# Kernel tuning notes

Measured on AMD Instinct MI355X. Metric: run time of the kernel, lower is better.

Reference implementation:

```python
import jax, jax.numpy as jnp
import numpy as np

SHIFT = 8  # shift_range init kwarg
EPS = 1e-12  # F.normalize default eps (x / max(||x||, eps))


def setup_inputs() -> dict:
    key = jax.random.key(0)
    k1, k2 = jax.random.split(key)
    grd_feature = jax.random.normal(k1, (64, 64, 24, 24), dtype=jnp.float32)
    sat_feature = jax.random.normal(k2, (64, 64, 64, 64), dtype=jnp.float32)
    return {"grd_feature": grd_feature, "sat_feature": sat_feature}


def reference(grd_feature, sat_feature):
    M, C, Hs, Ws = sat_feature.shape
    N, _, H, W = grd_feature.shape
    kH = min(H, Hs - 2 * SHIFT, 24)
    kW = min(W, Ws - 2 * SHIFT, 24)
    # center-crop ground features to kernel size
    grd = grd_feature[:, :, H // 2 - kH // 2: H // 2 + kH // 2,
                      W // 2 - kW // 2: W // 2 + kW // 2]  # [N,C,kH,kW]
    # crop sat features to search window (kernel + 2*shift)
    sat = sat_feature[:, :, Hs // 2 - SHIFT - kH // 2: Hs // 2 + SHIFT + kH // 2,
                      Ws // 2 - SHIFT - kW // 2: Ws // 2 + SHIFT + kW // 2]  # [M,C,Hi,Wi]
    # cross-correlation: repeat+grouped-conv in torch == plain conv2d here -> [M,N,Ho,Wo]
    corr = jax.lax.conv_general_dilated(
        sat, grd, window_strides=(1, 1), padding='VALID',
        dimension_numbers=('NCHW', 'OIHW', 'NCHW'))
    Ho, Wo = corr.shape[2], corr.shape[3]
    flat_idx = jnp.argmax(corr.reshape(M, N, Ho * Wo), axis=-1)  # [M,N]
    hy = flat_idx // Wo
    wx = flat_idx % Wo

    def gather_patch(sat_j, h, w):  # sat_j: [C,Hi,Wi]
        return jax.lax.dynamic_slice(sat_j, (0, h, w), (C, kH, kW))

    # vectorized patch gather over (M, N) -> [M,N,C,kH,kW]
    patches = jax.vmap(
        lambda sj, hs, ws: jax.vmap(lambda h, w: gather_patch(sj, h, w))(hs, ws)
    )(sat, hy, wx)

    pn = patches.reshape(M * N, -1)
    pn = pn / jnp.maximum(jnp.linalg.norm(pn, axis=-1, keepdims=True), EPS)
    pn = pn.reshape(M, N, C, kH, kW)
    gn = grd.reshape(N, -1)
    gn = gn / jnp.maximum(jnp.linalg.norm(gn, axis=-1, keepdims=True), EPS)
    gn = gn.reshape(N, C, kH, kW)
    similarity_matrix = jnp.einsum('mnchw,nchw->mn', pn, gn)
    sat_f = patches[M - 1, N - 1]  # last gathered (unnormalized) patch, as in torch
    return similarity_matrix, sat_f
```

## Files before the change

### kernel.cpp

```cpp
#include <hip/hip_runtime.h>
#include <hip/hip_bf16.h>
#include <math.h>


typedef float f32x16 __attribute__((ext_vector_type(16)));
typedef short short8 __attribute__((ext_vector_type(8)));

#define SATT_H 0u
#define GRDT_H 3276800u
#define CORR_O 4456448u
#define WING_O 5701632u
#define GN2_O  5702016u
#define CEX_O  5702080u
#define S2G_O  5702464u

__global__ __launch_bounds__(256) void make_satT(const float* __restrict__ sat,
                                                 __hip_bfloat16* __restrict__ sth,
                                                 float* __restrict__ S2g) {
    __shared__ __hip_bfloat16 th[40 * 66];
    int m = blockIdx.x / 40, r = blockIdx.x % 40;
    int tid = threadIdx.x;
    const float* base = sat + (size_t)m * 262144 + (12 + r) * 64 + 12;
    for (int k = 0; k < 10; k++) {
        int idx = tid + 256 * k;
        int c = idx / 40, w2 = idx % 40;
        th[w2 * 66 + c] = __float2bfloat16(base[c * 4096 + w2]);
    }
    __syncthreads();
    __hip_bfloat16* dh = sth + (size_t)m * 102400 + r * 640;
    for (int k = 0; k < 10; k++) {
        int idx = tid + 256 * k;
        int cc = idx / 640, rem = idx - cc * 640;
        int w2 = rem >> 4, cl = rem & 15;
        dh[cc * 25600 + w2 * 16 + cl] = th[w2 * 66 + cc * 16 + cl];
    }
    if (tid < 40) {
        float s = 0.0f;
        for (int c = 0; c < 64; c++) {
            float v = __bfloat162float(th[tid * 66 + c]);
            s += v * v;
        }
        S2g[m * 1600 + r * 40 + tid] = s;
    }
}

__global__ __launch_bounds__(256) void make_grdT(const float* __restrict__ grd,
                                                 __hip_bfloat16* __restrict__ gth,
                                                 float* __restrict__ gn2) {
    __shared__ __hip_bfloat16 t[32 * 577];
    __shared__ float red[4];
    int bid = blockIdx.x;
    int n = bid >> 1, ch = bid & 1;
    int tid = threadIdx.x;
    const float* src = grd + (size_t)n * 36864 + ch * 32 * 576;
    float s = 0.0f;
    for (int k = 0; k < 72; k++) {
        int idx = tid + 256 * k;
        int cl = idx / 576, ij = idx % 576;
        float v = src[idx];
        s += v * v;
        t[cl * 577 + ij] = __float2bfloat16(v);
    }
    for (int off = 32; off; off >>= 1) s += __shfl_down(s, off);
    if ((tid & 63) == 0) red[tid >> 6] = s;
    __syncthreads();
    if (tid == 0) atomicAdd(&gn2[n], red[0] + red[1] + red[2] + red[3]);
    for (int k = 0; k < 72; k++) {
        int idx = tid + 256 * k;
        int ij = idx >> 5, cl = idx & 31;
        int c = ch * 32 + cl;
        gth[((size_t)((c >> 4) * 576 + ij)) * 1024 + n * 16 + (c & 15)] = t[cl * 577 + ij];
    }
}

__global__ __launch_bounds__(256, 2) void corr_mfma(const __hip_bfloat16* __restrict__ sth,
                                                    const __hip_bfloat16* __restrict__ gth,
                                                    float* __restrict__ corr) {
    __shared__ __align__(16) __hip_bfloat16 satW[760 * 16];

    int bid = blockIdx.x;
    int xcd = bid & 7, slot = bid >> 3;
    int m = xcd * 8 + (slot >> 3), iq = slot & 7;
    int tid = threadIdx.x;
    int w = tid >> 6, l = tid & 63;
    int ln31 = l & 31, h = l >> 5;

    int rowbase[3];
#pragma unroll
    for (int t = 0; t < 3; t++) {
        int p = (w + 4 * t) * 32 + ln31;
        if (p > 288) p = 288;
        rowbase[t] = (p / 17) * 40 + (p % 17);
    }
    f32x16 acc[3][2];
#pragma unroll
    for (int t = 0; t < 3; t++) {
        acc[t][0] = (f32x16)0.0f;
        acc[t][1] = (f32x16)0.0f;
    }

    const __hip_bfloat16* gbase = gth + (size_t)(iq * 72) * 1024 + ln31 * 16 + h * 8;

#define BLOADR(B0, B1, CC, IJL) {                                               \
        const __hip_bfloat16* p_ = gbase + ((size_t)(CC) * 576 + (IJL)) * 1024; \
        B0 = *(const short8*)p_;                                                \
        B1 = *(const short8*)(p_ + 512);                                        \
    }
#define COMPUTE(IJL, B0, B1) {                                                  \
        int il_ = (IJL) / 24;                                                   \
        int pixoff_ = il_ * 40 + ((IJL) - il_ * 24);                            \
        if (w < 2) {                                                            \
            _Pragma("unroll")                                                   \
            for (int t = 0; t < 3; t++) {                                       \
                int ao = (rowbase[t] + pixoff_) * 32 + h * 16;                  \
                short8 af = *(const short8*)((const char*)satW + ao);           \
                acc[t][0] = __builtin_amdgcn_mfma_f32_32x32x16_bf16(af, B0, acc[t][0], 0, 0, 0); \
                acc[t][1] = __builtin_amdgcn_mfma_f32_32x32x16_bf16(af, B1, acc[t][1], 0, 0, 0); \
            }                                                                   \
        } else {                                                                \
            _Pragma("unroll")                                                   \
            for (int t = 0; t < 2; t++) {                                       \
                int ao = (rowbase[t] + pixoff_) * 32 + h * 16;                  \
                short8 af = *(const short8*)((const char*)satW + ao);           \
                acc[t][0] = __builtin_amdgcn_mfma_f32_32x32x16_bf16(af, B0, acc[t][0], 0, 0, 0); \
                acc[t][1] = __builtin_amdgcn_mfma_f32_32x32x16_bf16(af, B1, acc[t][1], 0, 0, 0); \
            }                                                                   \
        }                                                                       \
    }

#pragma unroll
    for (int cc = 0; cc < 4; cc++) {
        __syncthreads();
        const __hip_bfloat16* satb = sth + (size_t)m * 102400 + cc * 25600 + iq * 1920;
#pragma unroll
        for (int k2 = 0; k2 < 6; k2++) {
            int s = tid + 256 * k2;
            if (s < 1520) {
                float4 v = *(const float4*)(satb + s * 8);
                *(float4*)((char*)satW + s * 16) = v;
            }
        }
        short8 x0, x1, y0, y1, z0, z1;
        BLOADR(x0, x1, cc, 0);
        BLOADR(y0, y1, cc, 1);
        BLOADR(z0, z1, cc, 2);
        __syncthreads();

        for (int ijg = 0; ijg < 24; ijg++) {
            int base = ijg * 3;
            COMPUTE(base + 0, x0, x1);
            if (base + 3 < 72) BLOADR(x0, x1, cc, base + 3);
            COMPUTE(base + 1, y0, y1);
            if (base + 4 < 72) BLOADR(y0, y1, cc, base + 4);
            COMPUTE(base + 2, z0, z1);
            if (base + 5 < 72) BLOADR(z0, z1, cc, base + 5);
        }
    }

    int T = (w < 2) ? 3 : 2;
#pragma unroll
    for (int t = 0; t < 3; t++) {
        if (t >= T) break;
        int tile = w + 4 * t;
#pragma unroll
        for (int nt = 0; nt < 2; nt++)
#pragma unroll
            for (int q = 0; q < 16; q++) {
                int prow = tile * 32 + (q & 3) + 8 * (q >> 2) + 4 * h;
                if (prow < 289)
                    atomicAdd(&corr[((size_t)m * 304 + prow) * 64 + nt * 32 + ln31],
                              acc[t][nt][q]);
            }
    }
#undef BLOADR
#undef COMPUTE
}

__global__ __launch_bounds__(256) void argsim(const float* __restrict__ corr,
                                              const float* __restrict__ S2g,
                                              const float* __restrict__ gn2,
                                              float* __restrict__ winG,
                                              float* __restrict__ out) {
    __shared__ float S2[40][41];
    __shared__ float RS[40][18];
    __shared__ float w2[304];
    __shared__ float gn[64];
    __shared__ float fbv[4][64];
    __shared__ int   fbi[4][64];
    int m = blockIdx.x, tid = threadIdx.x;
    for (int k = 0; k < 7; k++) {
        int idx = tid + 256 * k;
        if (idx < 1600) S2[idx / 40][idx % 40] = S2g[m * 1600 + idx];
    }
    if (tid < 64) gn[tid] = gn2[tid];
    __syncthreads();
    for (int k = 0; k < 3; k++) {
        int idx = tid + 256 * k;
        if (idx < 680) {
            int r = idx / 17, x = idx % 17;
            float s = 0.0f;
            for (int j = 0; j < 24; j++) s += S2[r][x + j];
            RS[r][x] = s;
        }
    }
    __syncthreads();
    for (int k = 0; k < 2; k++) {
        int idx = tid + 256 * k;
        if (idx < 289) {
            int y = idx / 17, x = idx % 17;
            float s = 0.0f;
            for (int i2 = 0; i2 < 24; i2++) s += RS[y + i2][x];
            w2[idx] = s;
            if (m == 63) winG[idx] = s;
        }
    }
    __syncthreads();
    int n = tid & 63, pg = tid >> 6;
    float bv = -3.0e38f;
    int bi = 1 << 30;
    for (int p = pg; p < 289; p += 4) {
        float v = corr[((size_t)m * 304 + p) * 64 + n];
        if (v > bv) { bv = v; bi = p; }
    }
    fbv[pg][n] = bv;
    fbi[pg][n] = bi;
    __syncthreads();
    if (pg == 0) {
        for (int q = 1; q < 4; q++) {
            float ov = fbv[q][n];
            int oi = fbi[q][n];
            if (ov > bv || (ov == bv && oi < bi)) { bv = ov; bi = oi; }
        }
        out[m * 64 + n] = bv / (fmaxf(sqrtf(w2[bi]), 1e-12f) * fmaxf(sqrtf(gn[n]), 1e-12f));
    }
}

__global__ __launch_bounds__(256) void exact63(const float* __restrict__ sat,
                                               const float* __restrict__ grd,
                                               float* __restrict__ correx) {
    int p = blockIdx.x;
    int hy = p / 17, wx = p % 17;
    int tid = threadIdx.x;
    const float* satm = sat + (size_t)63 * 262144;
    const float* grdn = grd + (size_t)63 * 36864;
    float dot = 0.0f;
    for (int e = tid; e < 36864; e += 256) {
        int c = e / 576, rem = e - c * 576;
        int i = rem / 24, j = rem - i * 24;
        dot += satm[c * 4096 + (12 + hy + i) * 64 + 12 + wx + j] * grdn[e];
    }
    for (int off = 32; off; off >>= 1) dot += __shfl_down(dot, off);
    __shared__ float red[4];
    if ((tid & 63) == 0) red[tid >> 6] = dot;
    __syncthreads();
    if (tid == 0) correx[p] = red[0] + red[1] + red[2] + red[3];
}

__global__ __launch_bounds__(256) void copy_patch(const float* __restrict__ sat,
                                                  const float* __restrict__ cex,
                                                  const float* __restrict__ winG,
                                                  const float* __restrict__ gn2,
                                                  float* __restrict__ out) {
    __shared__ float rbv[4];
    __shared__ int rbi[4];
    int tid = threadIdx.x;
    float bv = -3.0e38f;
    int bi = 1 << 30;
    for (int p = tid; p < 289; p += 256) {
        float v = cex[p];
        if (v > bv) { bv = v; bi = p; }
    }
    for (int off = 32; off; off >>= 1) {
        float ov = __shfl_down(bv, off);
        int oi = __shfl_down(bi, off);
        if (ov > bv || (ov == bv && oi < bi)) { bv = ov; bi = oi; }
    }
    if ((tid & 63) == 0) { rbv[tid >> 6] = bv; rbi[tid >> 6] = bi; }
    __syncthreads();
    if (tid == 0) {
        for (int q = 1; q < 4; q++)
            if (rbv[q] > rbv[0] || (rbv[q] == rbv[0] && rbi[q] < rbi[0])) {
                rbv[0] = rbv[q]; rbi[0] = rbi[q];
            }
        if (blockIdx.x == 0)
            out[4095] = rbv[0] / (fmaxf(sqrtf(winG[rbi[0]]), 1e-12f) *
                                  fmaxf(sqrtf(gn2[63]), 1e-12f));
    }
    __syncthreads();
    int fidx = rbi[0];
    int hy = fidx / 17, wx = fidx % 17;
    int e = blockIdx.x * 256 + tid;
    int c = e / 576;
    int rem = e - c * 576;
    int rr = rem / 24, col = rem - rr * 24;
    out[4096 + e] = sat[(size_t)(63 * 64 + c) * 4096 + (12 + hy + rr) * 64 + 12 + wx + col];
}

extern "C" void kernel_launch(void* const* d_in, const int* in_sizes, int n_in,
                              void* d_out, int out_size, void* d_ws, size_t ws_size,
                              hipStream_t stream) {
    const float* grd = (const float*)d_in[0];
    const float* sat = (const float*)d_in[1];
    float* out = (float*)d_out;

    float* wsf = (float*)d_ws;
    __hip_bfloat16* sth = (__hip_bfloat16*)(wsf + SATT_H);
    __hip_bfloat16* gth = (__hip_bfloat16*)(wsf + GRDT_H);
    float* corr = wsf + CORR_O;
    float* winG = wsf + WING_O;
    float* gn2  = wsf + GN2_O;
    float* cex  = wsf + CEX_O;
    float* S2g  = wsf + S2G_O;

    hipMemsetAsync(corr, 0, (size_t)1245632 * sizeof(float), stream);
    make_satT<<<2560, 256, 0, stream>>>(sat, sth, S2g);
    make_grdT<<<128, 256, 0, stream>>>(grd, gth, gn2);
    corr_mfma<<<512, 256, 0, stream>>>(sth, gth, corr);
    argsim<<<64, 256, 0, stream>>>(corr, S2g, gn2, winG, out);
    exact63<<<289, 256, 0, stream>>>(sat, grd, cex);
    copy_patch<<<144, 256, 0, stream>>>(sat, cex, winG, gn2, out);
}
```

Baseline: 196.6 us.

## Fuse prep kernels with memset and exact63 into corr launch, add MFMA priority

```diff
diff --git a/kernel.cpp b/kernel.cpp
--- a/kernel.cpp
+++ b/kernel.cpp
@@ -11,77 +11,107 @@
 #define CORR_O 4456448u
 #define WING_O 5701632u
 #define GN2_O  5702016u
-#define CEX_O  5702080u
-#define S2G_O  5702464u
-
-__global__ __launch_bounds__(256) void make_satT(const float* __restrict__ sat,
-                                                 __hip_bfloat16* __restrict__ sth,
-                                                 float* __restrict__ S2g) {
-    __shared__ __hip_bfloat16 th[40 * 66];
-    int m = blockIdx.x / 40, r = blockIdx.x % 40;
+#define CEX_O  5702144u
+#define S2G_O  5702528u
+
+__global__ __launch_bounds__(256) void prep(const float* __restrict__ sat,
+                                            const float* __restrict__ grd,
+                                            __hip_bfloat16* __restrict__ sth,
+                                            __hip_bfloat16* __restrict__ gth,
+                                            float* __restrict__ S2g,
+                                            float* __restrict__ gn2p,
+                                            float* __restrict__ corrz) {
+    __shared__ __hip_bfloat16 shb[32 * 577];
+    int bid = blockIdx.x;
     int tid = threadIdx.x;
-    const float* base = sat + (size_t)m * 262144 + (12 + r) * 64 + 12;
-    for (int k = 0; k < 10; k++) {
-        int idx = tid + 256 * k;
-        int c = idx / 40, w2 = idx % 40;
-        th[w2 * 66 + c] = __float2bfloat16(base[c * 4096 + w2]);
-    }
-    __syncthreads();
-    __hip_bfloat16* dh = sth + (size_t)m * 102400 + r * 640;
-    for (int k = 0; k < 10; k++) {
-        int idx = tid + 256 * k;
-        int cc = idx / 640, rem = idx - cc * 640;
-        int w2 = rem >> 4, cl = rem & 15;
-        dh[cc * 25600 + w2 * 16 + cl] = th[w2 * 66 + cc * 16 + cl];
-    }
-    if (tid < 40) {
+
+    if (bid < 2560) {
+        {
+            int f4 = bid * 122 + tid;
+            if (tid < 122 && f4 < 311392)
+                ((float4*)corrz)[f4] = make_float4(0.f, 0.f, 0.f, 0.f);
+        }
+        int m = bid / 40, r = bid % 40;
+        const float* base = sat + (size_t)m * 262144 + (12 + r) * 64 + 12;
+        for (int k = 0; k < 10; k++) {
+            int idx = tid + 256 * k;
+            int c = idx / 40, w2 = idx % 40;
+            shb[w2 * 66 + c] = __float2bfloat16(base[c * 4096 + w2]);
+        }
+        __syncthreads();
+        __hip_bfloat16* dh = sth + (size_t)m * 102400 + r * 640;
+        for (int k = 0; k < 10; k++) {
+            int idx = tid + 256 * k;
+            int cc = idx / 640, rem = idx - cc * 640;
+            int w2 = rem >> 4, cl = rem & 15;
+            dh[cc * 25600 + w2 * 16 + cl] = shb[w2 * 66 + cc * 16 + cl];
+        }
+        if (tid < 40) {
+            float s = 0.0f;
+            for (int c = 0; c < 64; c++) {
+                float v = __bfloat162float(shb[tid * 66 + c]);
+                s += v * v;
+            }
+            S2g[m * 1600 + r * 40 + tid] = s;
+        }
+    } else {
+        __shared__ float red[4];
+        int x = bid - 2560;
+        int n = x >> 1, ch = x & 1;
+        const float* src = grd + (size_t)n * 36864 + ch * 32 * 576;
         float s = 0.0f;
-        for (int c = 0; c < 64; c++) {
-            float v = __bfloat162float(th[tid * 66 + c]);
+        for (int k = 0; k < 72; k++) {
+            int idx = tid + 256 * k;
+            int cl = idx / 576, ij = idx % 576;
+            float v = src[idx];
             s += v * v;
-        }
-        S2g[m * 1600 + r * 40 + tid] = s;
-    }
-}
-
-__global__ __launch_bounds__(256) void make_grdT(const float* __restrict__ grd,
-                                                 __hip_bfloat16* __restrict__ gth,
-                                                 float* __restrict__ gn2) {
-    __shared__ __hip_bfloat16 t[32 * 577];
-    __shared__ float red[4];
-    int bid = blockIdx.x;
-    int n = bid >> 1, ch = bid & 1;
-    int tid = threadIdx.x;
-    const float* src = grd + (size_t)n * 36864 + ch * 32 * 576;
-    float s = 0.0f;
-    for (int k = 0; k < 72; k++) {
-        int idx = tid + 256 * k;
-        int cl = idx / 576, ij = idx % 576;
-        float v = src[idx];
-        s += v * v;
-        t[cl * 577 + ij] = __float2bfloat16(v);
-    }
-    for (int off = 32; off; off >>= 1) s += __shfl_down(s, off);
-    if ((tid & 63) == 0) red[tid >> 6] = s;
-    __syncthreads();
-    if (tid == 0) atomicAdd(&gn2[n], red[0] + red[1] + red[2] + red[3]);
-    for (int k = 0; k < 72; k++) {
-        int idx = tid + 256 * k;
-        int ij = idx >> 5, cl = idx & 31;
-        int c = ch * 32 + cl;
-        gth[((size_t)((c >> 4) * 576 + ij)) * 1024 + n * 16 + (c & 15)] = t[cl * 577 + ij];
+            shb[cl * 577 + ij] = __float2bfloat16(v);
+        }
+        for (int off = 32; off; off >>= 1) s += __shfl_down(s, off);
+        if ((tid & 63) == 0) red[tid >> 6] = s;
+        __syncthreads();
+        if (tid == 0) gn2p[ch * 64 + n] = red[0] + red[1] + red[2] + red[3];
+        for (int k = 0; k < 72; k++) {
+            int idx = tid + 256 * k;
+            int ij = idx >> 5, cl = idx & 31;
+            int c = ch * 32 + cl;
+            gth[((size_t)((c >> 4) * 576 + ij)) * 1024 + n * 16 + (c & 15)] = shb[cl * 577 + ij];
+        }
     }
 }
 
 __global__ __launch_bounds__(256, 2) void corr_mfma(const __hip_bfloat16* __restrict__ sth,
                                                     const __hip_bfloat16* __restrict__ gth,
-                                                    float* __restrict__ corr) {
+                                                    float* __restrict__ corr,
+                                                    const float* __restrict__ sat,
+                                                    const float* __restrict__ grd,
+                                                    float* __restrict__ correx) {
     __shared__ __align__(16) __hip_bfloat16 satW[760 * 16];
 
     int bid = blockIdx.x;
+    int tid = threadIdx.x;
+
+    if (bid >= 512) {
+        int p = bid - 512;
+        int hy = p / 17, wx = p % 17;
+        const float* satm = sat + (size_t)63 * 262144;
+        const float* grdn = grd + (size_t)63 * 36864;
+        float dot = 0.0f;
+        for (int e = tid; e < 36864; e += 256) {
+            int c = e / 576, rem = e - c * 576;
+            int i = rem / 24, j = rem - i * 24;
+            dot += satm[c * 4096 + (12 + hy + i) * 64 + 12 + wx + j] * grdn[e];
+        }
+        for (int off = 32; off; off >>= 1) dot += __shfl_down(dot, off);
+        float* red = (float*)satW;
+        if ((tid & 63) == 0) red[tid >> 6] = dot;
+        __syncthreads();
+        if (tid == 0) correx[p] = red[0] + red[1] + red[2] + red[3];
+        return;
+    }
+
     int xcd = bid & 7, slot = bid >> 3;
     int m = xcd * 8 + (slot >> 3), iq = slot & 7;
-    int tid = threadIdx.x;
     int w = tid >> 6, l = tid & 63;
     int ln31 = l & 31, h = l >> 5;
 
@@ -109,6 +139,7 @@
 #define COMPUTE(IJL, B0, B1) {                                                  \
         int il_ = (IJL) / 24;                                                   \
         int pixoff_ = il_ * 40 + ((IJL) - il_ * 24);                            \
+        __builtin_amdgcn_s_setprio(1);                                          \
         if (w < 2) {                                                            \
             _Pragma("unroll")                                                   \
             for (int t = 0; t < 3; t++) {                                       \
@@ -126,6 +157,7 @@
                 acc[t][1] = __builtin_amdgcn_mfma_f32_32x32x16_bf16(af, B1, acc[t][1], 0, 0, 0); \
             }                                                                   \
         }                                                                       \
+        __builtin_amdgcn_s_setprio(0);                                          \
     }
 
 #pragma unroll
@@ -178,7 +210,7 @@
 
 __global__ __launch_bounds__(256) void argsim(const float* __restrict__ corr,
                                               const float* __restrict__ S2g,
-                                              const float* __restrict__ gn2,
+                                              const float* __restrict__ gn2p,
                                               float* __restrict__ winG,
                                               float* __restrict__ out) {
     __shared__ float S2[40][41];
@@ -192,7 +224,7 @@
         int idx = tid + 256 * k;
         if (idx < 1600) S2[idx / 40][idx % 40] = S2g[m * 1600 + idx];
     }
-    if (tid < 64) gn[tid] = gn2[tid];
+    if (tid < 64) gn[tid] = gn2p[tid] + gn2p[64 + tid];
     __syncthreads();
     for (int k = 0; k < 3; k++) {
         int idx = tid + 256 * k;
@@ -235,31 +267,10 @@
     }
 }
 
-__global__ __launch_bounds__(256) void exact63(const float* __restrict__ sat,
-                                               const float* __restrict__ grd,
-                                               float* __restrict__ correx) {
-    int p = blockIdx.x;
-    int hy = p / 17, wx = p % 17;
-    int tid = threadIdx.x;
-    const float* satm = sat + (size_t)63 * 262144;
-    const float* grdn = grd + (size_t)63 * 36864;
-    float dot = 0.0f;
-    for (int e = tid; e < 36864; e += 256) {
-        int c = e / 576, rem = e - c * 576;
-        int i = rem / 24, j = rem - i * 24;
-        dot += satm[c * 4096 + (12 + hy + i) * 64 + 12 + wx + j] * grdn[e];
-    }
-    for (int off = 32; off; off >>= 1) dot += __shfl_down(dot, off);
-    __shared__ float red[4];
-    if ((tid & 63) == 0) red[tid >> 6] = dot;
-    __syncthreads();
-    if (tid == 0) correx[p] = red[0] + red[1] + red[2] + red[3];
-}
-
 __global__ __launch_bounds__(256) void copy_patch(const float* __restrict__ sat,
                                                   const float* __restrict__ cex,
                                                   const float* __restrict__ winG,
-                                                  const float* __restrict__ gn2,
+                                                  const float* __restrict__ gn2p,
                                                   float* __restrict__ out) {
     __shared__ float rbv[4];
     __shared__ int rbi[4];
@@ -282,9 +293,11 @@
             if (rbv[q] > rbv[0] || (rbv[q] == rbv[0] && rbi[q] < rbi[0])) {
                 rbv[0] = rbv[q]; rbi[0] = rbi[q];
             }
-        if (blockIdx.x == 0)
+        if (blockIdx.x == 0) {
+            float gn63 = gn2p[63] + gn2p[127];
             out[4095] = rbv[0] / (fmaxf(sqrtf(winG[rbi[0]]), 1e-12f) *
-                                  fmaxf(sqrtf(gn2[63]), 1e-12f));
+                                  fmaxf(sqrtf(gn63), 1e-12f));
+        }
     }
     __syncthreads();
     int fidx = rbi[0];
@@ -308,15 +321,12 @@
     __hip_bfloat16* gth = (__hip_bfloat16*)(wsf + GRDT_H);
     float* corr = wsf + CORR_O;
     float* winG = wsf + WING_O;
-    float* gn2  = wsf + GN2_O;
+    float* gn2p = wsf + GN2_O;
     float* cex  = wsf + CEX_O;
     float* S2g  = wsf + S2G_O;
 
-    hipMemsetAsync(corr, 0, (size_t)1245632 * sizeof(float), stream);
-    make_satT<<<2560, 256, 0, stream>>>(sat, sth, S2g);
-    make_grdT<<<128, 256, 0, stream>>>(grd, gth, gn2);
-    corr_mfma<<<512, 256, 0, stream>>>(sth, gth, corr);
-    argsim<<<64, 256, 0, stream>>>(corr, S2g, gn2, winG, out);
-    exact63<<<289, 256, 0, stream>>>(sat, grd, cex);
-    copy_patch<<<144, 256, 0, stream>>>(sat, cex, winG, gn2, out);
-}
+    prep<<<2688, 256, 0, stream>>>(sat, grd, sth, gth, S2g, gn2p, corr);
+    corr_mfma<<<801, 256, 0, stream>>>(sth, gth, corr, sat, grd, cex);
+    argsim<<<64, 256, 0, stream>>>(corr, S2g, gn2p, winG, out);
+    copy_patch<<<144, 256, 0, stream>>>(sat, cex, winG, gn2p, out);
+}
```

After: 180.8 us. -8.0%, faster.
